# Kernel tuning notes

Hardware: AMD Instinct MI355X
Metric: run time of the kernel (lower is better)

## Reference

```python
import jax, jax.numpy as jnp
import numpy as np

B, T, C, H = 4, 2048, 1024, 16
D = C // H  # head dim = 64


def setup_inputs() -> dict:
    key = jax.random.key(0)
    k_x, k_wa, k_ba, k_wp, k_bp = jax.random.split(key, 5)
    s = 1.0 / np.sqrt(C)
    return {
        "x": jax.random.normal(k_x, (B, T, C), dtype=jnp.float32),
        "w_attn": jax.random.uniform(k_wa, (C, 3 * C), minval=-s, maxval=s, dtype=jnp.float32),
        "b_attn": jax.random.uniform(k_ba, (3 * C,), minval=-s, maxval=s, dtype=jnp.float32),
        "w_proj": jax.random.uniform(k_wp, (C, C), minval=-s, maxval=s, dtype=jnp.float32),
        "b_proj": jax.random.uniform(k_bp, (C,), minval=-s, maxval=s, dtype=jnp.float32),
    }


def reference(x, w_attn, b_attn, w_proj, b_proj):
    b, t, c = x.shape
    qkv = x @ w_attn + b_attn  # [b, t, 3c]
    q, k, v = jnp.split(qkv, 3, axis=-1)
    # [b, h, t, d]
    q = q.reshape(b, t, H, D).transpose(0, 2, 1, 3)
    k = k.reshape(b, t, H, D).transpose(0, 2, 1, 3)
    v = v.reshape(b, t, H, D).transpose(0, 2, 1, 3)
    scale = 1.0 / np.sqrt(D)
    logits = jnp.einsum("bhqd,bhkd->bhqk", q, k) * scale
    causal = jnp.tril(jnp.ones((t, t), dtype=bool))
    logits = jnp.where(causal, logits, jnp.finfo(logits.dtype).min)
    attn = jax.nn.softmax(logits, axis=-1)
    y = jnp.einsum("bhqk,bhkd->bhqd", attn, v)
    y = y.transpose(0, 2, 1, 3).reshape(b, t, c)
    return y @ w_proj + b_proj
```

## Files before the change

kernel.cpp:

```cpp
#include <hip/hip_runtime.h>


using u16 = unsigned short;
using u32 = unsigned int;
using bf16x8 = __attribute__((ext_vector_type(8))) __bf16;
using f32x4  = __attribute__((ext_vector_type(4))) float;
using f32x16 = __attribute__((ext_vector_type(16))) float;
using u16x8  = __attribute__((ext_vector_type(8))) u16;
using u16x4  = __attribute__((ext_vector_type(4))) u16;
using u32x2  = __attribute__((ext_vector_type(2))) u32;
using u32x4  = __attribute__((ext_vector_type(4))) u32;
using fvec4  = __attribute__((ext_vector_type(4))) float;

__device__ __forceinline__ u16 f2bf(float f) {
  u32 u = __builtin_bit_cast(u32, f);
  u32 r = (u + 0x7FFFu + ((u >> 16) & 1u)) >> 16;
  return (u16)r;
}

__device__ __forceinline__ u32 cvtpk(float lo, float hi) {
  u32 r;
  asm("v_cvt_pk_bf16_f32 %0, %1, %2" : "=v"(r) : "v"(lo), "v"(hi));
  return r;
}

__device__ __forceinline__ f32x4 mfma16(bf16x8 a, bf16x8 b, f32x4 c) {
  return __builtin_amdgcn_mfma_f32_16x16x32_bf16(a, b, c, 0, 0, 0);
}

__device__ __forceinline__ f32x16 mfma32(bf16x8 a, bf16x8 b, f32x16 c) {
  return __builtin_amdgcn_mfma_f32_32x32x16_bf16(a, b, c, 0, 0, 0);
}

__device__ __forceinline__ void gld16(const u16* g, u16* l) {
  __builtin_amdgcn_global_load_lds(
      (const __attribute__((address_space(1))) void*)g,
      (__attribute__((address_space(3))) void*)l, 16, 0, 0);
}

__global__ __launch_bounds__(256) void conv_kernel(
    const float* __restrict__ in, u16* __restrict__ out) {
  const size_t i = ((size_t)blockIdx.x * 256 + threadIdx.x) * 8;
  fvec4 a = *(const fvec4*)(in + i);
  fvec4 b = *(const fvec4*)(in + i + 4);
  u16x8 h;
#pragma unroll
  for (int j = 0; j < 4; ++j) { h[j] = f2bf(a[j]); h[4 + j] = f2bf(b[j]); }
  *(u16x8*)(out + i) = h;
}

__global__ __launch_bounds__(256) void transpose_conv_kernel(
    const float* __restrict__ W, u16* __restrict__ Wt, int K, int N) {
  __shared__ float tile[32][33];
  const int n0 = blockIdx.x * 32, k0 = blockIdx.y * 32;
  const int tx = threadIdx.x, ty = threadIdx.y;
#pragma unroll
  for (int j = 0; j < 4; ++j)
    tile[ty + j * 8][tx] = W[(size_t)(k0 + ty + j * 8) * N + n0 + tx];
  __syncthreads();
#pragma unroll
  for (int j = 0; j < 4; ++j)
    Wt[(size_t)(n0 + ty + j * 8) * K + k0 + tx] = f2bf(tile[tx][ty + j * 8]);
}

template <bool QKV>
__global__ __launch_bounds__(256) void gemm_kernel(
    const u16* __restrict__ A, const u16* __restrict__ Bt,
    const float* __restrict__ bias, void* __restrict__ Cp,
    u16* __restrict__ vt, int M, int N, int K) {
  constexpr float SC = 0.18033688011112042f;
  __shared__ u16 As[2][4096];
  __shared__ u16 Bs[2][4096];
  const int tid = threadIdx.x;
  const int l = tid & 63, w = tid >> 6;
  const int l15 = l & 15, l16 = l >> 4;
  const int wm = (w >> 1) * 64, wn = (w & 1) * 64;

  const u32 nwg = gridDim.x * gridDim.y;
  u32 f = blockIdx.y * gridDim.x + blockIdx.x;
  f = (f & 7) * (nwg >> 3) + (f >> 3);
  const long mbase = (long)(f / gridDim.x) * 128;
  const long nbase = (long)(f % gridDim.x) * 128;

  const int srow = tid >> 2;
  const int scol = ((tid & 3) ^ ((srow >> 1) & 3)) * 8;
  const u16* gA0 = A + (mbase + srow) * (long)K + scol;
  const u16* gA1 = gA0 + 64 * (long)K;
  const u16* gB0 = Bt + (nbase + srow) * (long)K + scol;
  const u16* gB1 = gB0 + 64 * (long)K;

  f32x4 acc[4][4] = {};
  const int NT = K >> 5;

#define STAGE(buf, koff)                         \
  gld16(gA0 + (koff), &As[buf][tid * 8]);        \
  gld16(gA1 + (koff), &As[buf][tid * 8 + 2048]); \
  gld16(gB0 + (koff), &Bs[buf][tid * 8]);        \
  gld16(gB1 + (koff), &Bs[buf][tid * 8 + 2048]);

  STAGE(0, 0);
  asm volatile("s_waitcnt vmcnt(0)" ::: "memory");
  __builtin_amdgcn_s_barrier();

  for (int t = 0; t < NT; ++t) {
    const int cur = t & 1;
    if (t + 1 < NT) { STAGE(cur ^ 1, (t + 1) * 32); }

    bf16x8 af[4], bfr[4];
#pragma unroll
    for (int i = 0; i < 4; ++i) {
      const int row = wm + i * 16 + l15;
      af[i] = *(const bf16x8*)(&As[cur][row * 32 + ((l16 ^ ((row >> 1) & 3)) * 8)]);
    }
#pragma unroll
    for (int j = 0; j < 4; ++j) {
      const int row = wn + j * 16 + l15;
      bfr[j] = *(const bf16x8*)(&Bs[cur][row * 32 + ((l16 ^ ((row >> 1) & 3)) * 8)]);
    }
    asm volatile("s_waitcnt lgkmcnt(0)" ::: "memory");
    __builtin_amdgcn_sched_barrier(0);
    __builtin_amdgcn_s_setprio(1);
#pragma unroll
    for (int i = 0; i < 4; ++i)
#pragma unroll
      for (int j = 0; j < 4; ++j)
        acc[i][j] = mfma16(af[i], bfr[j], acc[i][j]);
    __builtin_amdgcn_s_setprio(0);
    __builtin_amdgcn_sched_barrier(0);
    if (t + 1 < NT) { asm volatile("s_waitcnt vmcnt(0)" ::: "memory"); }
    __builtin_amdgcn_s_barrier();
  }
#undef STAGE

  if constexpr (QKV) {
    const bool isv = (nbase >= 2048);
#pragma unroll
    for (int i = 0; i < 4; ++i) {
#pragma unroll
      for (int j = 0; j < 4; ++j) {
        const long m0 = mbase + wm + i * 16 + l16 * 4;
        const int n = (int)nbase + wn + j * 16 + l15;
        const float bv = bias[n];
        if (!isv) {
          u16* qkp = (u16*)Cp;
          const float sc = (n < 1024) ? SC : 1.0f;
#pragma unroll
          for (int r = 0; r < 4; ++r)
            qkp[(m0 + r) * 2048 + n] = f2bf((acc[i][j][r] + bv) * sc);
        } else {
          const int vc = n - 2048, hh = vc >> 6, dd = vc & 63;
          const int bb = (int)(m0 >> 11), t0 = (int)(m0 & 2047);
          u16x4 pk;
#pragma unroll
          for (int r = 0; r < 4; ++r) pk[r] = f2bf(acc[i][j][r] + bv);
          *(u16x4*)(vt + ((size_t)(bb * 16 + hh) * 64 + dd) * 2048 + t0) = pk;
        }
      }
    }
  } else {
#pragma unroll
    for (int i = 0; i < 4; ++i) {
#pragma unroll
      for (int j = 0; j < 4; ++j) {
        const long row0 = mbase + wm + i * 16 + l16 * 4;
        const long col = nbase + wn + j * 16 + l15;
        const float bv = bias[col];
#pragma unroll
        for (int r = 0; r < 4; ++r)
          ((float*)Cp)[(row0 + r) * (long)N + col] = acc[i][j][r] + bv;
      }
    }
  }
}

__global__ __launch_bounds__(256, 2) void flash_kernel(
    const u16* __restrict__ qk, const u16* __restrict__ vt, u16* __restrict__ attn_out) {
  __shared__ u16 Ks[2][64 * 64];
  __shared__ u16 Vs[2][64 * 64];
  const int tid = threadIdx.x;
  const int lane = tid & 63, w = tid >> 6;
  const int l31 = lane & 31, hi = lane >> 5;
  const int xorv = (l31 & 7) << 4;

  const u32 i = blockIdx.y * 8 + blockIdx.x;
  const int jj = i >> 3;
  const int bh = (i & 7) | ((jj & 7) << 3);
  const int pair = (int)(i >> 6);
  const int b = bh >> 4, h = bh & 15;
  const u16* qbase = qk + (size_t)b * 2048 * 2048 + h * 64;
  const u16* kbase = qbase + 1024;
  const u16* vbase = vt + (size_t)bh * 64 * 2048;
  u16* obase = attn_out + (size_t)b * 2048 * 1024 + h * 64;

  const int sr = tid >> 3;
  const int ss = (tid & 7) ^ (sr & 7);
  const u16* gk = kbase + (size_t)sr * 2048 + ss * 8;
  const u16* gv = vbase + (size_t)sr * 2048 + ss * 8;

  int cur = 0;
  for (int half = 0; half < 2; ++half) {
    const int qt = half ? (15 - pair) : pair;
    const int nt = 2 * qt + 2;
    const int qr0 = qt * 128 + w * 32;
    const int q = qr0 + l31;
    const int ktmax = 2 * qt + (w >> 1);

    bf16x8 qf[4];
#pragma unroll
    for (int ds = 0; ds < 4; ++ds)
      qf[ds] = *(const bf16x8*)(qbase + (size_t)q * 2048 + ds * 16 + hi * 8);

    f32x16 oacc[2] = {};
    float lsum = 0.f;

    gld16(gk, &Ks[cur][tid * 8]);
    gld16(gk + (size_t)32 * 2048, &Ks[cur][tid * 8 + 2048]);
    gld16(gv, &Vs[cur][tid * 8]);
    gld16(gv + (size_t)32 * 2048, &Vs[cur][tid * 8 + 2048]);
    asm volatile("s_waitcnt vmcnt(0)" ::: "memory");
    __builtin_amdgcn_s_barrier();

    for (int kt = 0; kt < nt; ++kt) {
      const int kb = kt * 64;
      if (kt + 1 < nt) {
        gld16(gk + (size_t)(kb + 64) * 2048, &Ks[cur ^ 1][tid * 8]);
        gld16(gk + (size_t)(kb + 96) * 2048, &Ks[cur ^ 1][tid * 8 + 2048]);
        gld16(gv + (size_t)(kb + 64), &Vs[cur ^ 1][tid * 8]);
        gld16(gv + (size_t)32 * 2048 + (kb + 64), &Vs[cur ^ 1][tid * 8 + 2048]);
      }

      if (kt <= ktmax) {
        f32x16 s0 = {}, s1 = {};
        __builtin_amdgcn_s_setprio(1);
#pragma unroll
        for (int ds = 0; ds < 4; ++ds) {
          const int col = (ds * 32 + hi * 16) ^ xorv;
          bf16x8 k0 = *(const bf16x8*)((const char*)&Ks[cur][0] + l31 * 128 + col);
          bf16x8 k1 = *(const bf16x8*)((const char*)&Ks[cur][0] + (32 + l31) * 128 + col);
          s0 = mfma32(k0, qf[ds], s0);
          s1 = mfma32(k1, qf[ds], s1);
        }
        __builtin_amdgcn_s_setprio(0);

        if (kb + 63 > qr0) {
#pragma unroll
          for (int r = 0; r < 16; ++r) {
            const int crow = (r & 3) + 8 * (r >> 2) + 4 * hi;
            if (kb + crow > q) s0[r] = -1e30f;
            if (kb + 32 + crow > q) s1[r] = -1e30f;
          }
        }

        float p0[16], p1[16];
        float ps = 0.f;
#pragma unroll
        for (int r = 0; r < 16; ++r) {
          p0[r] = exp2f(s0[r]);
          p1[r] = exp2f(s1[r]);
          ps += p0[r] + p1[r];
        }
        lsum += ps;

        bf16x8 pf[4];
#pragma unroll
        for (int kh = 0; kh < 2; ++kh) {
#pragma unroll
          for (int c = 0; c < 2; ++c) {
            const float* pp = kh ? p1 : p0;
            const int bs = c * 8;
            u32 L0 = cvtpk(pp[bs + 0], pp[bs + 1]);
            u32 L1 = cvtpk(pp[bs + 2], pp[bs + 3]);
            u32 L2 = cvtpk(pp[bs + 4], pp[bs + 5]);
            u32 L3 = cvtpk(pp[bs + 6], pp[bs + 7]);
            asm("v_permlane32_swap_b32 %0, %1" : "+v"(L0), "+v"(L2));
            asm("v_permlane32_swap_b32 %0, %1" : "+v"(L1), "+v"(L3));
            u32x4 pk = {L0, L1, L2, L3};
            pf[kh * 2 + c] = __builtin_bit_cast(bf16x8, pk);
          }
        }

        __builtin_amdgcn_s_setprio(1);
#pragma unroll
        for (int dh = 0; dh < 2; ++dh)
#pragma unroll
          for (int ks = 0; ks < 4; ++ks) {
            const int col = (ks * 32 + hi * 16) ^ xorv;
            bf16x8 vf = *(const bf16x8*)((const char*)&Vs[cur][0] + (dh * 32 + l31) * 128 + col);
            oacc[dh] = mfma32(vf, pf[ks], oacc[dh]);
          }
        __builtin_amdgcn_s_setprio(0);
      }

      asm volatile("s_waitcnt vmcnt(0)" ::: "memory");
      __builtin_amdgcn_s_barrier();
      cur ^= 1;
    }

    lsum += __shfl_xor(lsum, 32);
    const float inv = 1.0f / lsum;
    u16* orow = obase + (size_t)q * 1024;
#pragma unroll
    for (int dh = 0; dh < 2; ++dh) {
#pragma unroll
      for (int jq = 0; jq < 4; ++jq) {
        u32x2 pk;
        pk[0] = cvtpk(oacc[dh][jq * 4 + 0] * inv, oacc[dh][jq * 4 + 1] * inv);
        pk[1] = cvtpk(oacc[dh][jq * 4 + 2] * inv, oacc[dh][jq * 4 + 3] * inv);
        *(u32x2*)(orow + dh * 32 + 8 * jq + 4 * hi) = pk;
      }
    }
  }
}

extern "C" void kernel_launch(void* const* d_in, const int* in_sizes, int n_in,
                              void* d_out, int out_size, void* d_ws, size_t ws_size,
                              hipStream_t stream) {
  (void)in_sizes; (void)n_in; (void)out_size; (void)ws_size;
  const float* x      = (const float*)d_in[0];
  const float* w_attn = (const float*)d_in[1];
  const float* b_attn = (const float*)d_in[2];
  const float* w_proj = (const float*)d_in[3];
  const float* b_proj = (const float*)d_in[4];
  float* out = (float*)d_out;

  char* ws = (char*)d_ws;
  u16* qkbuf = (u16*)(ws);
  u16* vtbuf = (u16*)(ws + 33554432);
  u16* xbf   = (u16*)(ws + 50331648);
  u16* attnb = (u16*)(ws + 50331648);
  u16* wtA   = (u16*)(ws + 67108864);
  u16* wtP   = (u16*)(ws + 73400320);

  conv_kernel<<<4096, 256, 0, stream>>>(x, xbf);
  transpose_conv_kernel<<<dim3(3072 / 32, 1024 / 32), dim3(32, 8), 0, stream>>>(w_attn, wtA, 1024, 3072);
  transpose_conv_kernel<<<dim3(1024 / 32, 1024 / 32), dim3(32, 8), 0, stream>>>(w_proj, wtP, 1024, 1024);

  gemm_kernel<true><<<dim3(3072 / 128, 8192 / 128), 256, 0, stream>>>(
      xbf, wtA, b_attn, qkbuf, vtbuf, 8192, 3072, 1024);

  flash_kernel<<<dim3(8, 64), 256, 0, stream>>>(qkbuf, vtbuf, attnb);

  gemm_kernel<false><<<dim3(1024 / 128, 8192 / 128), 256, 0, stream>>>(
      attnb, wtP, b_proj, out, nullptr, 8192, 1024, 1024);
}
```

Baseline: 178.5 us.

## Split flash kernel to one q-tile per block with finer causal skipping

```diff
diff --git a/kernel.cpp b/kernel.cpp
--- a/kernel.cpp
+++ b/kernel.cpp
@@ -173,7 +173,7 @@
   }
 }
 
-__global__ __launch_bounds__(256, 2) void flash_kernel(
+__global__ __launch_bounds__(256, 4) void flash_kernel(
     const u16* __restrict__ qk, const u16* __restrict__ vt, u16* __restrict__ attn_out) {
   __shared__ u16 Ks[2][64 * 64];
   __shared__ u16 Vs[2][64 * 64];
@@ -182,10 +182,11 @@
   const int l31 = lane & 31, hi = lane >> 5;
   const int xorv = (l31 & 7) << 4;
 
-  const u32 i = blockIdx.y * 8 + blockIdx.x;
-  const int jj = i >> 3;
-  const int bh = (i & 7) | ((jj & 7) << 3);
-  const int pair = (int)(i >> 6);
+  const int i = blockIdx.x;
+  const int bh = i & 63;
+  const int s = i >> 6;
+  const int g = s >> 2, j = s & 3;
+  const int qt = (g == 0) ? (15 - j) : (g == 1) ? j : (g == 2) ? (11 - j) : (4 + j);
   const int b = bh >> 4, h = bh & 15;
   const u16* qbase = qk + (size_t)b * 2048 * 2048 + h * 64;
   const u16* kbase = qbase + 1024;
@@ -197,117 +198,108 @@
   const u16* gk = kbase + (size_t)sr * 2048 + ss * 8;
   const u16* gv = vbase + (size_t)sr * 2048 + ss * 8;
 
+  const int nt = 2 * qt + 2;
+  const int qr0 = qt * 128 + w * 32;
+  const int q = qr0 + l31;
+  const int qmax = qr0 + 31;
+
+  bf16x8 qf[4];
+#pragma unroll
+  for (int ds = 0; ds < 4; ++ds)
+    qf[ds] = *(const bf16x8*)(qbase + (size_t)q * 2048 + ds * 16 + hi * 8);
+
+  f32x16 oacc[2] = {};
+  float lsum = 0.f;
+
+  gld16(gk, &Ks[0][tid * 8]);
+  gld16(gk + (size_t)32 * 2048, &Ks[0][tid * 8 + 2048]);
+  gld16(gv, &Vs[0][tid * 8]);
+  gld16(gv + (size_t)32 * 2048, &Vs[0][tid * 8 + 2048]);
+  asm volatile("s_waitcnt vmcnt(0)" ::: "memory");
+  __builtin_amdgcn_s_barrier();
+
   int cur = 0;
-  for (int half = 0; half < 2; ++half) {
-    const int qt = half ? (15 - pair) : pair;
-    const int nt = 2 * qt + 2;
-    const int qr0 = qt * 128 + w * 32;
-    const int q = qr0 + l31;
-    const int ktmax = 2 * qt + (w >> 1);
-
-    bf16x8 qf[4];
-#pragma unroll
-    for (int ds = 0; ds < 4; ++ds)
-      qf[ds] = *(const bf16x8*)(qbase + (size_t)q * 2048 + ds * 16 + hi * 8);
-
-    f32x16 oacc[2] = {};
-    float lsum = 0.f;
-
-    gld16(gk, &Ks[cur][tid * 8]);
-    gld16(gk + (size_t)32 * 2048, &Ks[cur][tid * 8 + 2048]);
-    gld16(gv, &Vs[cur][tid * 8]);
-    gld16(gv + (size_t)32 * 2048, &Vs[cur][tid * 8 + 2048]);
+  for (int kt = 0; kt < nt; ++kt) {
+    const int kb = kt * 64;
+    if (kt + 1 < nt) {
+      gld16(gk + (size_t)(kb + 64) * 2048, &Ks[cur ^ 1][tid * 8]);
+      gld16(gk + (size_t)(kb + 96) * 2048, &Ks[cur ^ 1][tid * 8 + 2048]);
+      gld16(gv + (size_t)(kb + 64), &Vs[cur ^ 1][tid * 8]);
+      gld16(gv + (size_t)32 * 2048 + (kb + 64), &Vs[cur ^ 1][tid * 8 + 2048]);
+    }
+
+    bf16x8 pf[4];
+#pragma unroll
+    for (int kh = 0; kh < 2; ++kh) {
+      const int kb32 = kb + kh * 32;
+      if (kb32 <= qmax) {
+        f32x16 sacc = {};
+        __builtin_amdgcn_s_setprio(1);
+#pragma unroll
+        for (int ds = 0; ds < 4; ++ds) {
+          const int col = (ds * 32 + hi * 16) ^ xorv;
+          bf16x8 kf = *(const bf16x8*)((const char*)&Ks[cur][0] + (kh * 32 + l31) * 128 + col);
+          sacc = mfma32(kf, qf[ds], sacc);
+        }
+        __builtin_amdgcn_s_setprio(0);
+
+        if (kb32 + 31 > qr0) {
+#pragma unroll
+          for (int r = 0; r < 16; ++r) {
+            const int key = kb32 + (r & 3) + 8 * (r >> 2) + 4 * hi;
+            if (key > q) sacc[r] = -1e30f;
+          }
+        }
+
+        float ps = 0.f;
+#pragma unroll
+        for (int r = 0; r < 16; ++r) { sacc[r] = exp2f(sacc[r]); ps += sacc[r]; }
+        lsum += ps;
+
+#pragma unroll
+        for (int c = 0; c < 2; ++c) {
+          const int bs = c * 8;
+          u32 L0 = cvtpk(sacc[bs + 0], sacc[bs + 1]);
+          u32 L1 = cvtpk(sacc[bs + 2], sacc[bs + 3]);
+          u32 L2 = cvtpk(sacc[bs + 4], sacc[bs + 5]);
+          u32 L3 = cvtpk(sacc[bs + 6], sacc[bs + 7]);
+          asm("v_permlane32_swap_b32 %0, %1" : "+v"(L0), "+v"(L2));
+          asm("v_permlane32_swap_b32 %0, %1" : "+v"(L1), "+v"(L3));
+          u32x4 pk = {L0, L1, L2, L3};
+          pf[kh * 2 + c] = __builtin_bit_cast(bf16x8, pk);
+        }
+      }
+    }
+
+    __builtin_amdgcn_s_setprio(1);
+#pragma unroll
+    for (int dh = 0; dh < 2; ++dh)
+#pragma unroll
+      for (int ks = 0; ks < 4; ++ks) {
+        if (kb + (ks >> 1) * 32 <= qmax) {
+          const int col = (ks * 32 + hi * 16) ^ xorv;
+          bf16x8 vf = *(const bf16x8*)((const char*)&Vs[cur][0] + (dh * 32 + l31) * 128 + col);
+          oacc[dh] = mfma32(vf, pf[ks], oacc[dh]);
+        }
+      }
+    __builtin_amdgcn_s_setprio(0);
+
     asm volatile("s_waitcnt vmcnt(0)" ::: "memory");
     __builtin_amdgcn_s_barrier();
-
-    for (int kt = 0; kt < nt; ++kt) {
-      const int kb = kt * 64;
-      if (kt + 1 < nt) {
-        gld16(gk + (size_t)(kb + 64) * 2048, &Ks[cur ^ 1][tid * 8]);
-        gld16(gk + (size_t)(kb + 96) * 2048, &Ks[cur ^ 1][tid * 8 + 2048]);
-        gld16(gv + (size_t)(kb + 64), &Vs[cur ^ 1][tid * 8]);
-        gld16(gv + (size_t)32 * 2048 + (kb + 64), &Vs[cur ^ 1][tid * 8 + 2048]);
-      }
-
-      if (kt <= ktmax) {
-        f32x16 s0 = {}, s1 = {};
-        __builtin_amdgcn_s_setprio(1);
-#pragma unroll
-        for (int ds = 0; ds < 4; ++ds) {
-          const int col = (ds * 32 + hi * 16) ^ xorv;
-          bf16x8 k0 = *(const bf16x8*)((const char*)&Ks[cur][0] + l31 * 128 + col);
-          bf16x8 k1 = *(const bf16x8*)((const char*)&Ks[cur][0] + (32 + l31) * 128 + col);
-          s0 = mfma32(k0, qf[ds], s0);
-          s1 = mfma32(k1, qf[ds], s1);
-        }
-        __builtin_amdgcn_s_setprio(0);
-
-        if (kb + 63 > qr0) {
-#pragma unroll
-          for (int r = 0; r < 16; ++r) {
-            const int crow = (r & 3) + 8 * (r >> 2) + 4 * hi;
-            if (kb + crow > q) s0[r] = -1e30f;
-            if (kb + 32 + crow > q) s1[r] = -1e30f;
-          }
-        }
-
-        float p0[16], p1[16];
-        float ps = 0.f;
-#pragma unroll
-        for (int r = 0; r < 16; ++r) {
-          p0[r] = exp2f(s0[r]);
-          p1[r] = exp2f(s1[r]);
-          ps += p0[r] + p1[r];
-        }
-        lsum += ps;
-
-        bf16x8 pf[4];
-#pragma unroll
-        for (int kh = 0; kh < 2; ++kh) {
-#pragma unroll
-          for (int c = 0; c < 2; ++c) {
-            const float* pp = kh ? p1 : p0;
-            const int bs = c * 8;
-            u32 L0 = cvtpk(pp[bs + 0], pp[bs + 1]);
-            u32 L1 = cvtpk(pp[bs + 2], pp[bs + 3]);
-            u32 L2 = cvtpk(pp[bs + 4], pp[bs + 5]);
-            u32 L3 = cvtpk(pp[bs + 6], pp[bs + 7]);
-            asm("v_permlane32_swap_b32 %0, %1" : "+v"(L0), "+v"(L2));
-            asm("v_permlane32_swap_b32 %0, %1" : "+v"(L1), "+v"(L3));
-            u32x4 pk = {L0, L1, L2, L3};
-            pf[kh * 2 + c] = __builtin_bit_cast(bf16x8, pk);
-          }
-        }
-
-        __builtin_amdgcn_s_setprio(1);
-#pragma unroll
-        for (int dh = 0; dh < 2; ++dh)
-#pragma unroll
-          for (int ks = 0; ks < 4; ++ks) {
-            const int col = (ks * 32 + hi * 16) ^ xorv;
-            bf16x8 vf = *(const bf16x8*)((const char*)&Vs[cur][0] + (dh * 32 + l31) * 128 + col);
-            oacc[dh] = mfma32(vf, pf[ks], oacc[dh]);
-          }
-        __builtin_amdgcn_s_setprio(0);
-      }
-
-      asm volatile("s_waitcnt vmcnt(0)" ::: "memory");
-      __builtin_amdgcn_s_barrier();
-      cur ^= 1;
-    }
-
-    lsum += __shfl_xor(lsum, 32);
-    const float inv = 1.0f / lsum;
-    u16* orow = obase + (size_t)q * 1024;
-#pragma unroll
-    for (int dh = 0; dh < 2; ++dh) {
-#pragma unroll
-      for (int jq = 0; jq < 4; ++jq) {
-        u32x2 pk;
-        pk[0] = cvtpk(oacc[dh][jq * 4 + 0] * inv, oacc[dh][jq * 4 + 1] * inv);
-        pk[1] = cvtpk(oacc[dh][jq * 4 + 2] * inv, oacc[dh][jq * 4 + 3] * inv);
-        *(u32x2*)(orow + dh * 32 + 8 * jq + 4 * hi) = pk;
-      }
+    cur ^= 1;
+  }
+
+  lsum += __shfl_xor(lsum, 32);
+  const float inv = 1.0f / lsum;
+  u16* orow = obase + (size_t)q * 1024;
+#pragma unroll
+  for (int dh = 0; dh < 2; ++dh) {
+#pragma unroll
+    for (int jq = 0; jq < 4; ++jq) {
+      u32x2 pk;
+      pk[0] = cvtpk(oacc[dh][jq * 4 + 0] * inv, oacc[dh][jq * 4 + 1] * inv);
+      pk[1] = cvtpk(oacc[dh][jq * 4 + 2] * inv, oacc[dh][jq * 4 + 3] * inv);
+      *(u32x2*)(orow + dh * 32 + 8 * jq + 4 * hi) = pk;
     }
   }
 }
@@ -338,7 +330,7 @@
   gemm_kernel<true><<<dim3(3072 / 128, 8192 / 128), 256, 0, stream>>>(
       xbf, wtA, b_attn, qkbuf, vtbuf, 8192, 3072, 1024);
 
-  flash_kernel<<<dim3(8, 64), 256, 0, stream>>>(qkbuf, vtbuf, attnb);
+  flash_kernel<<<1024, 256, 0, stream>>>(qkbuf, vtbuf, attnb);
 
   gemm_kernel<false><<<dim3(1024 / 128, 8192 / 128), 256, 0, stream>>>(
       attnb, wtP, b_proj, out, nullptr, 8192, 1024, 1024);
```

New measurement: 288.5 us. 1.62x slower.
